# Kernel optimization log

Measured on AMD Instinct MI355X. Metric: run time of the kernel, lower is better.

## Reference

```python
import jax, jax.numpy as jnp
import numpy as np

NUM_FEATURE = 50


def setup_inputs() -> dict:
    key = jax.random.key(0)
    k1, k2 = jax.random.split(key)
    query = jax.random.normal(k1, (512, NUM_FEATURE), dtype=jnp.float32)
    doc = jax.random.normal(k2, (512, 256, NUM_FEATURE), dtype=jnp.float32)
    # nn.Linear(150, 1, bias=False) with weight filled with 1
    W = jnp.ones((3 * NUM_FEATURE,), dtype=jnp.float32)
    return {"query": query, "doc": doc, "W": W}


def reference(query, doc, W):
    # Split the single 150-dim linear weight into the three trilinear parts:
    # score(x, y) = w1.sen_x + w2.q_y + w3.(sen_x * q_y)
    w1, w2, w3 = W[:NUM_FEATURE], W[NUM_FEATURE:2 * NUM_FEATURE], W[2 * NUM_FEATURE:]
    q_term = query @ w2                      # [Lq]
    qw3 = query * w3                         # [Lq, d]

    def per_sentence(sen):                   # sen: [Ls, d]
        sXY = (sen @ w1)[:, None] + q_term[None, :] + sen @ qw3.T   # [Ls, Lq]
        sD2Q = jax.nn.softmax(sXY, axis=0)   # softmax over sentence tokens
        sQ2D = jax.nn.softmax(sXY, axis=1)   # softmax over query tokens
        aD2Q = sD2Q @ query                  # [Ls, d]
        aQ2D = sD2Q @ (sQ2D.T @ sen)         # (sD2Q @ sQ2D.T) @ sen, cheaper order
        return jnp.concatenate([sen, aD2Q, sen * aD2Q, sen * aQ2D], axis=1)  # [Ls, 4d]

    return jax.vmap(per_sentence)(doc)       # [n_sen, Ls, 4d]
```

## Files before the change

kernel.cpp:

```cpp
#include <hip/hip_runtime.h>
#include <math.h>

typedef __bf16 bf16_t;
typedef bf16_t bf16x2 __attribute__((ext_vector_type(2)));
typedef bf16_t bf16x4 __attribute__((ext_vector_type(4)));
typedef bf16_t bf16x8 __attribute__((ext_vector_type(8)));
typedef float f32x4 __attribute__((ext_vector_type(4)));

#define MFMA16(a,b,c) __builtin_amdgcn_mfma_f32_16x16x32_bf16((a),(b),(c),0,0,0)

#define ND 256
#define NQ 512
#define NF 50
#define L2E 1.44269504f
#define SHIFT 64.0f

#define SENT_E 0
#define PD_E   16896
#define PQ_E   35328
#define TT_E   52224
#define QW3_E  61440
#define QTT_E  70656
#define STATS_B 150528
#define PART_B  70656
#define LDS_BYTES 155648

#define ST_QTERM 0
#define ST_CINV  512
#define ST_RINV  1024

__launch_bounds__(1024, 1)
__global__ void ca3_kernel(const float* __restrict__ query,
                           const float* __restrict__ doc,
                           const float* __restrict__ W,
                           float* __restrict__ out)
{
    extern __shared__ char smem[];
    bf16_t* lb = (bf16_t*)smem;
    float* stats = (float*)(smem + STATS_B);
    float* part  = (float*)(smem + PART_B);

    const int tid = threadIdx.x;
    const int w = tid >> 6, l = tid & 63, ln = l & 15, lg = l >> 4;
    const int s = blockIdx.x;
    const float* sen_g = doc + (size_t)s * (ND * NF);

    for (int e = tid; e < 14 * 264; e += 1024) {
        int f = e / 264, i = e - f * 264;
        lb[SENT_E + (50 + f) * 264 + i] = (bf16_t)0.f;
    }
    for (int e = tid; e < 256 * 12; e += 1024) {
        int i = e / 12, f = e - i * 12;
        lb[PD_E + i * 72 + 52 + f] = (bf16_t)0.f;
    }
    for (int e = tid; e < 2 * 64 * 12; e += 1024) {
        int b = e / 768, r2 = e - b * 768;
        int jj = r2 / 12, f = 52 + (r2 - jj * 12);
        lb[QW3_E + b * 4608 + jj * 72 + f] = (bf16_t)0.f;
    }
    for (int e = tid; e < 14 * 72; e += 1024) {
        int f = e / 72, j = e - f * 72;
        lb[QTT_E + (50 + f) * 72 + j] = (bf16_t)0.f;
    }
    for (int e = tid; e < 256 * 25; e += 1024) {
        int i = e / 25, c = e - i * 25;
        float2 v = ((const float2*)sen_g)[i * 25 + c];
        bf16x2 p; p[0] = (bf16_t)v.x; p[1] = (bf16_t)v.y;
        *(bf16x2*)&lb[PD_E + i * 72 + 2 * c] = p;
        lb[SENT_E + (2 * c) * 264 + i]     = p[0];
        lb[SENT_E + (2 * c + 1) * 264 + i] = p[1];
    }
    if (tid < NQ) {
        float acc = 0.f;
        #pragma unroll
        for (int c = 0; c < 25; ++c) {
            float2 v = ((const float2*)query)[tid * 25 + c];
            acc += v.x * W[NF + 2 * c] + v.y * W[NF + 2 * c + 1];
        }
        stats[ST_QTERM + tid] = acc;
    }
    if (tid < ND) {
        float acc = 0.f;
        #pragma unroll
        for (int f = 0; f < NF; ++f) acc += sen_g[tid * NF + f] * W[f];
        lb[PD_E + tid * 72 + 50] = (bf16_t)1.0f;
        lb[PD_E + tid * 72 + 51] = (bf16_t)acc;
    }
    __syncthreads();

    bf16x8 aS[2];
    #pragma unroll
    for (int ks = 0; ks < 2; ++ks)
        aS[ks] = *(bf16x8*)&lb[PD_E + (w * 16 + ln) * 72 + lg * 8 + ks * 32];

    auto stageQW3 = [&](int jt, int buf) {
        const int j0 = jt * 64;
        bf16_t* dst = lb + QW3_E + buf * 4608;
        for (int e = tid; e < 1600; e += 1024) {
            int jj = e / 25, c = e - jj * 25;
            float2 v = ((const float2*)query)[(j0 + jj) * 25 + c];
            bf16x2 p;
            p[0] = (bf16_t)(v.x * W[2 * NF + 2 * c] * L2E);
            p[1] = (bf16_t)(v.y * W[2 * NF + 2 * c + 1] * L2E);
            *(bf16x2*)&dst[jj * 72 + 2 * c] = p;
        }
        if (tid < 64) {
            dst[tid * 72 + 50] = (bf16_t)(stats[ST_QTERM + j0 + tid] * L2E);
            dst[tid * 72 + 51] = (bf16_t)L2E;
        }
    };
    auto stageQTT = [&](int jt) {
        const int j0 = jt * 64;
        for (int e = tid; e < 1600; e += 1024) {
            int c = e >> 6, jj = e & 63;
            float ci = stats[ST_CINV + j0 + jj];
            float2 v = ((const float2*)query)[(j0 + jj) * 25 + c];
            lb[QTT_E + (2 * c) * 72 + jj]     = (bf16_t)(v.x * ci);
            lb[QTT_E + (2 * c + 1) * 72 + jj] = (bf16_t)(v.y * ci);
        }
    };

    float rpart[4] = {0.f, 0.f, 0.f, 0.f};
    stageQW3(0, 0);
    __syncthreads();

    for (int jt = 0; jt < 8; ++jt) {
        if (jt < 7) stageQW3(jt + 1, (jt + 1) & 1);
        const bf16_t* qb = lb + QW3_E + (jt & 1) * 4608;
        f32x4 acc[4];
        #pragma unroll
        for (int nf = 0; nf < 4; ++nf) acc[nf] = (f32x4){-SHIFT, -SHIFT, -SHIFT, -SHIFT};
        #pragma unroll
        for (int ks = 0; ks < 2; ++ks)
            #pragma unroll
            for (int nf = 0; nf < 4; ++nf) {
                bf16x8 b = *(bf16x8*)&qb[(nf * 16 + ln) * 72 + lg * 8 + ks * 32];
                acc[nf] = MFMA16(aS[ks], b, acc[nf]);
            }
        #pragma unroll
        for (int nf = 0; nf < 4; ++nf) {
            float e0 = exp2f(acc[nf][0]), e1 = exp2f(acc[nf][1]);
            float e2 = exp2f(acc[nf][2]), e3 = exp2f(acc[nf][3]);
            rpart[0] += e0; rpart[1] += e1; rpart[2] += e2; rpart[3] += e3;
            float c = (e0 + e1) + (e2 + e3);
            c += __shfl_xor(c, 16);
            c += __shfl_xor(c, 32);
            if (lg == 0) part[jt * 1024 + w * 64 + nf * 16 + ln] = c;
        }
        __syncthreads();
    }
    #pragma unroll
    for (int r = 0; r < 4; ++r) {
        float v = rpart[r];
        v += __shfl_xor(v, 1);
        v += __shfl_xor(v, 2);
        v += __shfl_xor(v, 4);
        v += __shfl_xor(v, 8);
        if (ln == 0) stats[ST_RINV + w * 16 + lg * 4 + r] = 1.f / v;
    }
    __syncthreads();
    if (tid < 512) {
        const float* pp = part + (tid >> 6) * 1024 + (tid & 63);
        float ssum = 0.f;
        #pragma unroll
        for (int ww = 0; ww < 16; ++ww) ssum += pp[ww * 64];
        stats[ST_CINV + tid] = 1.f / ssum;
    }
    {
        const int i = tid & 255;
        const float rv = stats[ST_RINV + i];
        for (int f = tid >> 8; f < 50; f += 4)
            lb[SENT_E + f * 264 + i] = (bf16_t)((float)lb[SENT_E + f * 264 + i] * rv);
    }
    __syncthreads();

    f32x4 accD[4], accQ[4];
    #pragma unroll
    for (int nf = 0; nf < 4; ++nf) {
        accD[nf] = (f32x4){0.f, 0.f, 0.f, 0.f};
        accQ[nf] = (f32x4){0.f, 0.f, 0.f, 0.f};
    }
    bf16x8 aP[2];
    const int mt = w & 3, nt = w >> 2;

    stageQW3(0, 0);
    __syncthreads();

    for (int jt = 0; jt < 8; ++jt) {
        if (jt > 0) {
            const bf16_t* tt = lb + TT_E + ((jt - 1) & 1) * 4608;
            #pragma unroll
            for (int ks = 0; ks < 2; ++ks)
                #pragma unroll
                for (int nf = 0; nf < 4; ++nf) {
                    bf16x8 bt = *(bf16x8*)&tt[(nf * 16 + ln) * 72 + lg * 8 + ks * 32];
                    accQ[nf] = MFMA16(aP[ks], bt, accQ[nf]);
                }
        }
        if (jt < 7) stageQW3(jt + 1, (jt + 1) & 1);
        stageQTT(jt);
        const bf16_t* qb = lb + QW3_E + (jt & 1) * 4608;
        f32x4 acc[4];
        #pragma unroll
        for (int nf = 0; nf < 4; ++nf) acc[nf] = (f32x4){-SHIFT, -SHIFT, -SHIFT, -SHIFT};
        #pragma unroll
        for (int ks = 0; ks < 2; ++ks)
            #pragma unroll
            for (int nf = 0; nf < 4; ++nf) {
                bf16x8 b = *(bf16x8*)&qb[(nf * 16 + ln) * 72 + lg * 8 + ks * 32];
                acc[nf] = MFMA16(aS[ks], b, acc[nf]);
            }
        #pragma unroll
        for (int nf = 0; nf < 4; ++nf) {
            bf16x4 pk;
            pk[0] = (bf16_t)exp2f(acc[nf][0]);
            pk[1] = (bf16_t)exp2f(acc[nf][1]);
            pk[2] = (bf16_t)exp2f(acc[nf][2]);
            pk[3] = (bf16_t)exp2f(acc[nf][3]);
            *(bf16x4*)&lb[PQ_E + (nf * 16 + ln) * 264 + w * 16 + lg * 4] = pk;
            #pragma unroll
            for (int r = 0; r < 4; ++r)
                lb[PD_E + (w * 16 + lg * 4 + r) * 72 + nf * 16 + ln] = pk[r];
        }
        __syncthreads();

        f32x4 tacc = (f32x4){0.f, 0.f, 0.f, 0.f};
        #pragma unroll
        for (int ks = 0; ks < 8; ++ks) {
            bf16x8 a = *(bf16x8*)&lb[PQ_E + (mt * 16 + ln) * 264 + lg * 8 + ks * 32];
            bf16x8 b = *(bf16x8*)&lb[SENT_E + (nt * 16 + ln) * 264 + lg * 8 + ks * 32];
            tacc = MFMA16(a, b, tacc);
        }
        bf16x4 tk;
        #pragma unroll
        for (int r = 0; r < 4; ++r)
            tk[r] = (bf16_t)(tacc[r] * stats[ST_CINV + jt * 64 + mt * 16 + lg * 4 + r]);
        *(bf16x4*)&lb[TT_E + (jt & 1) * 4608 + (nt * 16 + ln) * 72 + mt * 16 + lg * 4] = tk;

        #pragma unroll
        for (int ks = 0; ks < 2; ++ks) {
            aP[ks] = *(bf16x8*)&lb[PD_E + (w * 16 + ln) * 72 + lg * 8 + ks * 32];
            #pragma unroll
            for (int nf = 0; nf < 4; ++nf) {
                bf16x8 bq = *(bf16x8*)&lb[QTT_E + (nf * 16 + ln) * 72 + lg * 8 + ks * 32];
                accD[nf] = MFMA16(aP[ks], bq, accD[nf]);
            }
        }
        __syncthreads();
    }
    {
        const bf16_t* tt = lb + TT_E + 4608;
        #pragma unroll
        for (int ks = 0; ks < 2; ++ks)
            #pragma unroll
            for (int nf = 0; nf < 4; ++nf) {
                bf16x8 bt = *(bf16x8*)&tt[(nf * 16 + ln) * 72 + lg * 8 + ks * 32];
                accQ[nf] = MFMA16(aP[ks], bt, accQ[nf]);
            }
    }
    __syncthreads();

    float* ea = (float*)smem;
    float* eb = (float*)(smem + 69632);
    #pragma unroll
    for (int nf = 0; nf < 4; ++nf)
        #pragma unroll
        for (int r = 0; r < 4; ++r) {
            ea[(w * 16 + lg * 4 + r) * 68 + nf * 16 + ln] = accD[nf][r];
            eb[(w * 16 + lg * 4 + r) * 68 + nf * 16 + ln] = accQ[nf][r];
        }
    __syncthreads();
    const size_t ob0 = (size_t)s * (ND * 200);
    for (int v = tid; v < 25600; v += 1024) {
        int i = v / 100;
        int p = v - i * 100;
        int seg = p / 25;
        int f = (p - seg * 25) * 2;
        float2 o;
        if (seg == 0) {
            o = *(const float2*)&sen_g[i * 50 + f];
        } else if (seg == 1) {
            o.x = ea[i * 68 + f]; o.y = ea[i * 68 + f + 1];
        } else if (seg == 2) {
            float2 d = *(const float2*)&sen_g[i * 50 + f];
            o.x = d.x * ea[i * 68 + f]; o.y = d.y * ea[i * 68 + f + 1];
        } else {
            float2 d = *(const float2*)&sen_g[i * 50 + f];
            o.x = d.x * eb[i * 68 + f]; o.y = d.y * eb[i * 68 + f + 1];
        }
        *(float2*)&out[ob0 + (size_t)i * 200 + seg * 50 + f] = o;
    }
}

extern "C" void kernel_launch(void* const* d_in, const int* in_sizes, int n_in,
                              void* d_out, int out_size, void* d_ws, size_t ws_size,
                              hipStream_t stream) {
    const float* query = (const float*)d_in[0];
    const float* doc   = (const float*)d_in[1];
    const float* W     = (const float*)d_in[2];
    float* out = (float*)d_out;
    (void)d_ws; (void)ws_size; (void)n_in; (void)in_sizes; (void)out_size;

    hipFuncSetAttribute((const void*)ca3_kernel,
                        hipFuncAttributeMaxDynamicSharedMemorySize,
                        LDS_BYTES);
    ca3_kernel<<<dim3(512), dim3(1024), LDS_BYTES, stream>>>(query, doc, W, out);
}
```

Measured before the change: 151.7 us.

## Fuse two passes into one by accumulating symmetric D2Q·Q2Dᵀ kernel in registers

The kernel previously ran two sweeps over query tiles: one for the column and row softmax statistics, and one that recomputed the scores to build the D2Q and Q2D attentions. It now does a single sweep. Exp-scores are scaled by rsqrt of each query column's sum, so the Ls×Ls product sD2Q·sQ2Dᵀ can be built as P·Pᵀ and accumulated in 16 register tiles, with the row normalisation applied afterwards. This removes the recomputation of scores and the exponentials of the second pass. It adds extra barriers per tile, a 256×256 Gram accumulation per block, and higher register pressure, and it also moves staging work to warps 1–15 and reorders the output writes by segment.

```diff
diff --git a/kernel.cpp b/kernel.cpp
--- a/kernel.cpp
+++ b/kernel.cpp
@@ -16,117 +16,128 @@
 #define SHIFT 64.0f
 
 #define SENT_E 0
-#define PD_E   16896
-#define PQ_E   35328
-#define TT_E   52224
-#define QW3_E  61440
-#define QTT_E  70656
-#define STATS_B 150528
-#define PART_B  70656
-#define LDS_BYTES 155648
+#define PD0_E  17152
+#define PD1_E  35584
+#define QW3_E  54016
+#define QTT_E  63232
+#define KL0_E  17152
+#define KL1_E  27392
+#define PART_B  135680
+#define STATS_B 139776
+#define LDS_BYTES 143104
 
 #define ST_QTERM 0
-#define ST_CINV  512
-#define ST_RINV  1024
+#define ST_SQCI  512
+#define ST_RINV  576
 
 __launch_bounds__(1024, 1)
-__global__ void ca3_kernel(const float* __restrict__ query,
+__global__ void ca6_kernel(const float* __restrict__ query,
                            const float* __restrict__ doc,
                            const float* __restrict__ W,
                            float* __restrict__ out)
 {
     extern __shared__ char smem[];
     bf16_t* lb = (bf16_t*)smem;
+    float* part  = (float*)(smem + PART_B);
     float* stats = (float*)(smem + STATS_B);
-    float* part  = (float*)(smem + PART_B);
 
     const int tid = threadIdx.x;
     const int w = tid >> 6, l = tid & 63, ln = l & 15, lg = l >> 4;
     const int s = blockIdx.x;
     const float* sen_g = doc + (size_t)s * (ND * NF);
 
-    for (int e = tid; e < 14 * 264; e += 1024) {
-        int f = e / 264, i = e - f * 264;
-        lb[SENT_E + (50 + f) * 264 + i] = (bf16_t)0.f;
-    }
-    for (int e = tid; e < 256 * 12; e += 1024) {
-        int i = e / 12, f = e - i * 12;
-        lb[PD_E + i * 72 + 52 + f] = (bf16_t)0.f;
-    }
-    for (int e = tid; e < 2 * 64 * 12; e += 1024) {
-        int b = e / 768, r2 = e - b * 768;
-        int jj = r2 / 12, f = 52 + (r2 - jj * 12);
-        lb[QW3_E + b * 4608 + jj * 72 + f] = (bf16_t)0.f;
-    }
-    for (int e = tid; e < 14 * 72; e += 1024) {
-        int f = e / 72, j = e - f * 72;
-        lb[QTT_E + (50 + f) * 72 + j] = (bf16_t)0.f;
-    }
-    for (int e = tid; e < 256 * 25; e += 1024) {
-        int i = e / 25, c = e - i * 25;
-        float2 v = ((const float2*)sen_g)[i * 25 + c];
-        bf16x2 p; p[0] = (bf16_t)v.x; p[1] = (bf16_t)v.y;
-        *(bf16x2*)&lb[PD_E + i * 72 + 2 * c] = p;
-        lb[SENT_E + (2 * c) * 264 + i]     = p[0];
-        lb[SENT_E + (2 * c + 1) * 264 + i] = p[1];
-    }
-    if (tid < NQ) {
-        float acc = 0.f;
-        #pragma unroll
-        for (int c = 0; c < 25; ++c) {
-            float2 v = ((const float2*)query)[tid * 25 + c];
-            acc += v.x * W[NF + 2 * c] + v.y * W[NF + 2 * c + 1];
-        }
-        stats[ST_QTERM + tid] = acc;
-    }
-    if (tid < ND) {
-        float acc = 0.f;
-        #pragma unroll
-        for (int f = 0; f < NF; ++f) acc += sen_g[tid * NF + f] * W[f];
-        lb[PD_E + tid * 72 + 50] = (bf16_t)1.0f;
-        lb[PD_E + tid * 72 + 51] = (bf16_t)acc;
-    }
-    __syncthreads();
-
-    bf16x8 aS[2];
-    #pragma unroll
-    for (int ks = 0; ks < 2; ++ks)
-        aS[ks] = *(bf16x8*)&lb[PD_E + (w * 16 + ln) * 72 + lg * 8 + ks * 32];
-
-    auto stageQW3 = [&](int jt, int buf) {
+    auto stageQW3 = [&](int jt, int buf, int tbase, int tn) {
         const int j0 = jt * 64;
         bf16_t* dst = lb + QW3_E + buf * 4608;
-        for (int e = tid; e < 1600; e += 1024) {
-            int jj = e / 25, c = e - jj * 25;
-            float2 v = ((const float2*)query)[(j0 + jj) * 25 + c];
-            bf16x2 p;
-            p[0] = (bf16_t)(v.x * W[2 * NF + 2 * c] * L2E);
-            p[1] = (bf16_t)(v.y * W[2 * NF + 2 * c + 1] * L2E);
-            *(bf16x2*)&dst[jj * 72 + 2 * c] = p;
-        }
-        if (tid < 64) {
-            dst[tid * 72 + 50] = (bf16_t)(stats[ST_QTERM + j0 + tid] * L2E);
-            dst[tid * 72 + 51] = (bf16_t)L2E;
+        for (int e = tid - tbase; e < 1664; e += tn) {
+            int jj = e / 26, c = e - jj * 26;
+            if (c < 25) {
+                float2 v = ((const float2*)query)[(j0 + jj) * 25 + c];
+                bf16x2 p;
+                p[0] = (bf16_t)(v.x * W[100 + 2 * c] * L2E);
+                p[1] = (bf16_t)(v.y * W[100 + 2 * c + 1] * L2E);
+                *(bf16x2*)&dst[jj * 72 + 2 * c] = p;
+            } else {
+                bf16x2 p;
+                p[0] = (bf16_t)(stats[ST_QTERM + j0 + jj] * L2E);
+                p[1] = (bf16_t)L2E;
+                *(bf16x2*)&dst[jj * 72 + 50] = p;
+            }
         }
     };
     auto stageQTT = [&](int jt) {
         const int j0 = jt * 64;
         for (int e = tid; e < 1600; e += 1024) {
             int c = e >> 6, jj = e & 63;
-            float ci = stats[ST_CINV + j0 + jj];
+            float sq = stats[ST_SQCI + jj];
             float2 v = ((const float2*)query)[(j0 + jj) * 25 + c];
-            lb[QTT_E + (2 * c) * 72 + jj]     = (bf16_t)(v.x * ci);
-            lb[QTT_E + (2 * c + 1) * 72 + jj] = (bf16_t)(v.y * ci);
+            lb[QTT_E + (2 * c) * 72 + jj]     = (bf16_t)(v.x * sq);
+            lb[QTT_E + (2 * c + 1) * 72 + jj] = (bf16_t)(v.y * sq);
         }
     };
 
+    for (int e = tid; e < 938; e += 1024) {
+        int f = 50 + e / 67, c4 = (e - (e / 67) * 67) * 4;
+        *(bf16x4*)&lb[SENT_E + f * 268 + c4] = (bf16x4){(bf16_t)0.f,(bf16_t)0.f,(bf16_t)0.f,(bf16_t)0.f};
+    }
+    for (int e = tid; e < 768; e += 1024) {
+        int i = e / 3, c4 = 52 + (e - (e / 3) * 3) * 4;
+        *(bf16x4*)&lb[PD0_E + i * 72 + c4] = (bf16x4){(bf16_t)0.f,(bf16_t)0.f,(bf16_t)0.f,(bf16_t)0.f};
+    }
+    for (int e = tid; e < 384; e += 1024) {
+        int b = e / 192, r = e - b * 192;
+        int jj = r / 3, c4 = 52 + (r - (r / 3) * 3) * 4;
+        *(bf16x4*)&lb[QW3_E + b * 4608 + jj * 72 + c4] = (bf16x4){(bf16_t)0.f,(bf16_t)0.f,(bf16_t)0.f,(bf16_t)0.f};
+    }
+    for (int e = tid; e < 252; e += 1024) {
+        int f = 50 + e / 18, c4 = (e - (e / 18) * 18) * 4;
+        *(bf16x4*)&lb[QTT_E + f * 72 + c4] = (bf16x4){(bf16_t)0.f,(bf16_t)0.f,(bf16_t)0.f,(bf16_t)0.f};
+    }
+    for (int e = tid; e < 256 * 25; e += 1024) {
+        int i = e / 25, c = e - i * 25;
+        float2 v = ((const float2*)sen_g)[i * 25 + c];
+        bf16x2 p; p[0] = (bf16_t)v.x; p[1] = (bf16_t)v.y;
+        *(bf16x2*)&lb[PD0_E + i * 72 + 2 * c] = p;
+        lb[SENT_E + (2 * c) * 268 + i]     = p[0];
+        lb[SENT_E + (2 * c + 1) * 268 + i] = p[1];
+    }
+    if (tid < NQ) {
+        float acc = 0.f;
+        #pragma unroll
+        for (int c = 0; c < 25; ++c) {
+            float2 v = ((const float2*)query)[tid * 25 + c];
+            acc += v.x * W[NF + 2 * c] + v.y * W[NF + 2 * c + 1];
+        }
+        stats[ST_QTERM + tid] = acc;
+    }
+    if (tid < ND) {
+        float acc = 0.f;
+        #pragma unroll
+        for (int f = 0; f < NF; ++f) acc += sen_g[tid * NF + f] * W[f];
+        lb[PD0_E + tid * 72 + 50] = (bf16_t)1.0f;
+        lb[PD0_E + tid * 72 + 51] = (bf16_t)acc;
+    }
+    __syncthreads();
+
+    bf16x8 aS[2];
+    #pragma unroll
+    for (int ks = 0; ks < 2; ++ks)
+        aS[ks] = *(bf16x8*)&lb[PD0_E + (w * 16 + ln) * 72 + lg * 8 + ks * 32];
+    stageQW3(0, 0, 0, 1024);
+    __syncthreads();
+
+    f32x4 accD[4];
+    f32x4 K[16];
+    #pragma unroll
+    for (int nf = 0; nf < 4; ++nf) accD[nf] = (f32x4){0.f, 0.f, 0.f, 0.f};
+    #pragma unroll
+    for (int ib = 0; ib < 16; ++ib) K[ib] = (f32x4){0.f, 0.f, 0.f, 0.f};
     float rpart[4] = {0.f, 0.f, 0.f, 0.f};
-    stageQW3(0, 0);
-    __syncthreads();
 
     for (int jt = 0; jt < 8; ++jt) {
-        if (jt < 7) stageQW3(jt + 1, (jt + 1) & 1);
         const bf16_t* qb = lb + QW3_E + (jt & 1) * 4608;
+        bf16_t* pd = lb + ((jt & 1) ? PD1_E : PD0_E);
+
         f32x4 acc[4];
         #pragma unroll
         for (int nf = 0; nf < 4; ++nf) acc[nf] = (f32x4){-SHIFT, -SHIFT, -SHIFT, -SHIFT};
@@ -137,18 +148,61 @@
                 bf16x8 b = *(bf16x8*)&qb[(nf * 16 + ln) * 72 + lg * 8 + ks * 32];
                 acc[nf] = MFMA16(aS[ks], b, acc[nf]);
             }
+
+        float ev[4][4];
         #pragma unroll
         for (int nf = 0; nf < 4; ++nf) {
-            float e0 = exp2f(acc[nf][0]), e1 = exp2f(acc[nf][1]);
-            float e2 = exp2f(acc[nf][2]), e3 = exp2f(acc[nf][3]);
-            rpart[0] += e0; rpart[1] += e1; rpart[2] += e2; rpart[3] += e3;
-            float c = (e0 + e1) + (e2 + e3);
-            c += __shfl_xor(c, 16);
-            c += __shfl_xor(c, 32);
-            if (lg == 0) part[jt * 1024 + w * 64 + nf * 16 + ln] = c;
-        }
-        __syncthreads();
-    }
+            #pragma unroll
+            for (int r = 0; r < 4; ++r) {
+                ev[nf][r] = exp2f(acc[nf][r]);
+                rpart[r] += ev[nf][r];
+            }
+            float cp = (ev[nf][0] + ev[nf][1]) + (ev[nf][2] + ev[nf][3]);
+            cp += __shfl_xor(cp, 16);
+            cp += __shfl_xor(cp, 32);
+            if (lg == 0) part[w * 64 + nf * 16 + ln] = cp;
+        }
+        __syncthreads();
+
+        if (w == 0) {
+            float cs = 0.f;
+            #pragma unroll
+            for (int ww = 0; ww < 16; ++ww) cs += part[ww * 64 + l];
+            stats[ST_SQCI + l] = rsqrtf(cs);
+        } else if (jt < 7) {
+            stageQW3(jt + 1, (jt + 1) & 1, 64, 960);
+        }
+        __syncthreads();
+
+        #pragma unroll
+        for (int nf = 0; nf < 4; ++nf) {
+            float sq = stats[ST_SQCI + nf * 16 + ln];
+            #pragma unroll
+            for (int r = 0; r < 4; ++r)
+                pd[(w * 16 + lg * 4 + r) * 72 + nf * 16 + ln] = (bf16_t)(ev[nf][r] * sq);
+        }
+        stageQTT(jt);
+        __syncthreads();
+
+        bf16x8 aP[2];
+        #pragma unroll
+        for (int ks = 0; ks < 2; ++ks) {
+            aP[ks] = *(bf16x8*)&pd[(w * 16 + ln) * 72 + lg * 8 + ks * 32];
+            #pragma unroll
+            for (int nf = 0; nf < 4; ++nf) {
+                bf16x8 bq = *(bf16x8*)&lb[QTT_E + (nf * 16 + ln) * 72 + lg * 8 + ks * 32];
+                accD[nf] = MFMA16(aP[ks], bq, accD[nf]);
+            }
+        }
+        #pragma unroll
+        for (int ib = 0; ib < 16; ++ib)
+            #pragma unroll
+            for (int ks = 0; ks < 2; ++ks) {
+                bf16x8 bb = *(bf16x8*)&pd[(ib * 16 + ln) * 72 + lg * 8 + ks * 32];
+                K[ib] = MFMA16(aP[ks], bb, K[ib]);
+            }
+    }
+
     #pragma unroll
     for (int r = 0; r < 4; ++r) {
         float v = rpart[r];
@@ -159,104 +213,28 @@
         if (ln == 0) stats[ST_RINV + w * 16 + lg * 4 + r] = 1.f / v;
     }
     __syncthreads();
-    if (tid < 512) {
-        const float* pp = part + (tid >> 6) * 1024 + (tid & 63);
-        float ssum = 0.f;
-        #pragma unroll
-        for (int ww = 0; ww < 16; ++ww) ssum += pp[ww * 64];
-        stats[ST_CINV + tid] = 1.f / ssum;
-    }
-    {
-        const int i = tid & 255;
-        const float rv = stats[ST_RINV + i];
-        for (int f = tid >> 8; f < 50; f += 4)
-            lb[SENT_E + f * 264 + i] = (bf16_t)((float)lb[SENT_E + f * 264 + i] * rv);
-    }
-    __syncthreads();
-
-    f32x4 accD[4], accQ[4];
-    #pragma unroll
-    for (int nf = 0; nf < 4; ++nf) {
-        accD[nf] = (f32x4){0.f, 0.f, 0.f, 0.f};
-        accQ[nf] = (f32x4){0.f, 0.f, 0.f, 0.f};
-    }
-    bf16x8 aP[2];
-    const int mt = w & 3, nt = w >> 2;
-
-    stageQW3(0, 0);
-    __syncthreads();
-
-    for (int jt = 0; jt < 8; ++jt) {
-        if (jt > 0) {
-            const bf16_t* tt = lb + TT_E + ((jt - 1) & 1) * 4608;
-            #pragma unroll
-            for (int ks = 0; ks < 2; ++ks)
-                #pragma unroll
-                for (int nf = 0; nf < 4; ++nf) {
-                    bf16x8 bt = *(bf16x8*)&tt[(nf * 16 + ln) * 72 + lg * 8 + ks * 32];
-                    accQ[nf] = MFMA16(aP[ks], bt, accQ[nf]);
-                }
-        }
-        if (jt < 7) stageQW3(jt + 1, (jt + 1) & 1);
-        stageQTT(jt);
-        const bf16_t* qb = lb + QW3_E + (jt & 1) * 4608;
-        f32x4 acc[4];
-        #pragma unroll
-        for (int nf = 0; nf < 4; ++nf) acc[nf] = (f32x4){-SHIFT, -SHIFT, -SHIFT, -SHIFT};
-        #pragma unroll
-        for (int ks = 0; ks < 2; ++ks)
-            #pragma unroll
-            for (int nf = 0; nf < 4; ++nf) {
-                bf16x8 b = *(bf16x8*)&qb[(nf * 16 + ln) * 72 + lg * 8 + ks * 32];
-                acc[nf] = MFMA16(aS[ks], b, acc[nf]);
-            }
+
+    f32x4 accQ[4];
+    #pragma unroll
+    for (int nf = 0; nf < 4; ++nf) accQ[nf] = (f32x4){0.f, 0.f, 0.f, 0.f};
+    #pragma unroll
+    for (int kt = 0; kt < 8; ++kt) {
+        bf16_t* kl = lb + ((kt & 1) ? KL1_E : KL0_E);
+        #pragma unroll
+        for (int h = 0; h < 2; ++h) {
+            const int ib = 2 * kt + h;
+            float riv = stats[ST_RINV + ib * 16 + ln];
+            #pragma unroll
+            for (int r = 0; r < 4; ++r)
+                kl[(w * 16 + lg * 4 + r) * 40 + h * 16 + ln] = (bf16_t)(K[ib][r] * riv);
+        }
+        __syncthreads();
+        bf16x8 aK = *(bf16x8*)&kl[(w * 16 + ln) * 40 + lg * 8];
         #pragma unroll
         for (int nf = 0; nf < 4; ++nf) {
-            bf16x4 pk;
-            pk[0] = (bf16_t)exp2f(acc[nf][0]);
-            pk[1] = (bf16_t)exp2f(acc[nf][1]);
-            pk[2] = (bf16_t)exp2f(acc[nf][2]);
-            pk[3] = (bf16_t)exp2f(acc[nf][3]);
-            *(bf16x4*)&lb[PQ_E + (nf * 16 + ln) * 264 + w * 16 + lg * 4] = pk;
-            #pragma unroll
-            for (int r = 0; r < 4; ++r)
-                lb[PD_E + (w * 16 + lg * 4 + r) * 72 + nf * 16 + ln] = pk[r];
-        }
-        __syncthreads();
-
-        f32x4 tacc = (f32x4){0.f, 0.f, 0.f, 0.f};
-        #pragma unroll
-        for (int ks = 0; ks < 8; ++ks) {
-            bf16x8 a = *(bf16x8*)&lb[PQ_E + (mt * 16 + ln) * 264 + lg * 8 + ks * 32];
-            bf16x8 b = *(bf16x8*)&lb[SENT_E + (nt * 16 + ln) * 264 + lg * 8 + ks * 32];
-            tacc = MFMA16(a, b, tacc);
-        }
-        bf16x4 tk;
-        #pragma unroll
-        for (int r = 0; r < 4; ++r)
-            tk[r] = (bf16_t)(tacc[r] * stats[ST_CINV + jt * 64 + mt * 16 + lg * 4 + r]);
-        *(bf16x4*)&lb[TT_E + (jt & 1) * 4608 + (nt * 16 + ln) * 72 + mt * 16 + lg * 4] = tk;
-
-        #pragma unroll
-        for (int ks = 0; ks < 2; ++ks) {
-            aP[ks] = *(bf16x8*)&lb[PD_E + (w * 16 + ln) * 72 + lg * 8 + ks * 32];
-            #pragma unroll
-            for (int nf = 0; nf < 4; ++nf) {
-                bf16x8 bq = *(bf16x8*)&lb[QTT_E + (nf * 16 + ln) * 72 + lg * 8 + ks * 32];
-                accD[nf] = MFMA16(aP[ks], bq, accD[nf]);
-            }
-        }
-        __syncthreads();
-    }
-    {
-        const bf16_t* tt = lb + TT_E + 4608;
-        #pragma unroll
-        for (int ks = 0; ks < 2; ++ks)
-            #pragma unroll
-            for (int nf = 0; nf < 4; ++nf) {
-                bf16x8 bt = *(bf16x8*)&tt[(nf * 16 + ln) * 72 + lg * 8 + ks * 32];
-                accQ[nf] = MFMA16(aP[ks], bt, accQ[nf]);
-            }
+            bf16x8 b = *(bf16x8*)&lb[SENT_E + (nf * 16 + ln) * 268 + kt * 32 + lg * 8];
+            accQ[nf] = MFMA16(aK, b, accQ[nf]);
+        }
     }
     __syncthreads();
 
@@ -271,24 +249,25 @@
         }
     __syncthreads();
     const size_t ob0 = (size_t)s * (ND * 200);
-    for (int v = tid; v < 25600; v += 1024) {
-        int i = v / 100;
-        int p = v - i * 100;
-        int seg = p / 25;
-        int f = (p - seg * 25) * 2;
-        float2 o;
-        if (seg == 0) {
-            o = *(const float2*)&sen_g[i * 50 + f];
-        } else if (seg == 1) {
-            o.x = ea[i * 68 + f]; o.y = ea[i * 68 + f + 1];
-        } else if (seg == 2) {
-            float2 d = *(const float2*)&sen_g[i * 50 + f];
-            o.x = d.x * ea[i * 68 + f]; o.y = d.y * ea[i * 68 + f + 1];
-        } else {
-            float2 d = *(const float2*)&sen_g[i * 50 + f];
-            o.x = d.x * eb[i * 68 + f]; o.y = d.y * eb[i * 68 + f + 1];
-        }
-        *(float2*)&out[ob0 + (size_t)i * 200 + seg * 50 + f] = o;
+    #pragma unroll
+    for (int seg = 0; seg < 4; ++seg) {
+        for (int v = tid; v < 6400; v += 1024) {
+            int i = v / 25, c = v - (v / 25) * 25;
+            int f = 2 * c;
+            float2 o;
+            if (seg == 0) {
+                o = *(const float2*)&sen_g[i * 50 + f];
+            } else if (seg == 1) {
+                o.x = ea[i * 68 + f]; o.y = ea[i * 68 + f + 1];
+            } else if (seg == 2) {
+                float2 d = *(const float2*)&sen_g[i * 50 + f];
+                o.x = d.x * ea[i * 68 + f]; o.y = d.y * ea[i * 68 + f + 1];
+            } else {
+                float2 d = *(const float2*)&sen_g[i * 50 + f];
+                o.x = d.x * eb[i * 68 + f]; o.y = d.y * eb[i * 68 + f + 1];
+            }
+            *(float2*)&out[ob0 + (size_t)i * 200 + seg * 50 + f] = o;
+        }
     }
 }
 
@@ -301,8 +280,8 @@
     float* out = (float*)d_out;
     (void)d_ws; (void)ws_size; (void)n_in; (void)in_sizes; (void)out_size;
 
-    hipFuncSetAttribute((const void*)ca3_kernel,
+    hipFuncSetAttribute((const void*)ca6_kernel,
                         hipFuncAttributeMaxDynamicSharedMemorySize,
                         LDS_BYTES);
-    ca3_kernel<<<dim3(512), dim3(1024), LDS_BYTES, stream>>>(query, doc, W, out);
+    ca6_kernel<<<dim3(512), dim3(1024), LDS_BYTES, stream>>>(query, doc, W, out);
 }
```

After: 209.1 us. 37.8% more time.
